# Kernel optimization log

Hardware: AMD Instinct MI355X
Metric: run time of the kernel (lower is better)

Reference implementation:

```python
import jax, jax.numpy as jnp
import numpy as np

B, T, D = 8, 2048, 1024          # batch, seq_len, inp_dim
NH, DH = 8, 128                  # head_num, head_dim
H = NH * DH                      # hidden_dim = 1024
P = int((4.0 / 3.0) * H)         # proj_dim = 1365
EPS = 1e-6
CAP = 15.0                       # soft cap for i/f gate pre-activations


def setup_inputs() -> dict:
    key = jax.random.key(0)
    ks = jax.random.split(key, 32)
    r = lambda k, s, sc=0.02: jax.random.normal(k, s, jnp.float32) * sc
    return {
        "x": jax.random.normal(ks[0], (B, T, D), jnp.float32),
        "ln_w": jnp.ones((D,), jnp.float32),
        "ln_b": jnp.zeros((D,), jnp.float32),
        "hln_w": jnp.ones((H,), jnp.float32),
        "hln_b": jnp.zeros((H,), jnp.float32),
        "Wz": r(ks[1], (D, H)), "bz": r(ks[2], (H,)),
        "Wi": r(ks[3], (D, H)), "bi": r(ks[4], (H,)),
        "Wo": r(ks[5], (D, H)), "bo": r(ks[6], (H,)),
        "Wf": r(ks[7], (D, H)), "bf": r(ks[8], (H,)),
        "Rz": r(ks[9], (NH, DH, DH)), "rbz": r(ks[10], (H,)),
        "Ri": r(ks[11], (NH, DH, DH)), "rbi": r(ks[12], (H,)),
        "Ro": r(ks[13], (NH, DH, DH)), "rbo": r(ks[14], (H,)),
        "Rf": r(ks[15], (NH, DH, DH)), "rbf": r(ks[16], (H,)),
        "up_w": r(ks[17], (H, 2 * P)), "up_b": r(ks[18], (2 * P,)),
        "down_w": r(ks[19], (P, D)), "down_b": r(ks[20], (D,)),
    }


def _layernorm(v, w, b):
    mu = jnp.mean(v, axis=-1, keepdims=True)
    var = jnp.mean((v - mu) ** 2, axis=-1, keepdims=True)
    return (v - mu) * jax.lax.rsqrt(var + EPS) * w + b


def _soft_cap(v):
    return CAP * jnp.tanh(v / CAP)


def _block_linear(h, R, rb):
    # block-diagonal linear: h (B,H) -> per-head (B,NH,DH) @ (NH,DH,DH)
    hh = h.reshape(h.shape[0], NH, DH)
    return jnp.einsum('bhd,hde->bhe', hh, R).reshape(h.shape[0], H) + rb


def _multihead_layernorm(h, w, b):
    hh = h.reshape(h.shape[0], NH, DH)
    mu = jnp.mean(hh, axis=-1, keepdims=True)
    var = jnp.mean((hh - mu) ** 2, axis=-1, keepdims=True)
    normed = (hh - mu) * jax.lax.rsqrt(var + EPS)
    return normed.reshape(h.shape[0], H) * w + b


def reference(x, ln_w, ln_b, hln_w, hln_b,
              Wz, bz, Wi, bi, Wo, bo, Wf, bf,
              Rz, rbz, Ri, rbi, Ro, rbo, Rf, rbf,
              up_w, up_b, down_w, down_b):
    # use_conv=False path: x_c == x_t == LayerNorm(x)
    x_n = _layernorm(x, ln_w, ln_b)                       # (B,T,D)
    # precompute all input projections as large GEMMs
    zx = jnp.einsum('btd,dh->bth', x_n, Wz) + bz
    ix = jnp.einsum('btd,dh->bth', x_n, Wi) + bi
    ox = jnp.einsum('btd,dh->bth', x_n, Wo) + bo
    fx = jnp.einsum('btd,dh->bth', x_n, Wf) + bf

    tm = lambda a: jnp.transpose(a, (1, 0, 2))            # time-major
    xs = (tm(zx), tm(ix), tm(ox), tm(fx), tm(x))

    c0 = jnp.zeros((x.shape[0], H), jnp.float32)
    n0 = jnp.ones((x.shape[0], H), jnp.float32)
    h0 = jnp.zeros((x.shape[0], H), jnp.float32)
    m0 = jnp.zeros((x.shape[0], H), jnp.float32)

    def step(carry, inp_t):
        c, n, h, m = carry
        zx_t, ix_t, ox_t, fx_t, xres_t = inp_t
        i_pre = _soft_cap(ix_t + _block_linear(h, Ri, rbi))
        f_pre = _soft_cap(fx_t + _block_linear(h, Rf, rbf))
        z = jnp.tanh(zx_t + _block_linear(h, Rz, rbz))
        o = jax.nn.sigmoid(ox_t + _block_linear(h, Ro, rbo))
        m_t = jnp.maximum(f_pre + m, i_pre)
        i_g = jnp.exp(i_pre - m_t)
        f_g = jnp.exp(f_pre - m_t + m)
        c_t = f_g * c + i_g * z
        n_t = f_g * n + i_g
        h_t = o * (c_t / jnp.maximum(n_t, 1.0))
        out = _multihead_layernorm(h_t, hln_w, hln_b)
        u = out @ up_w + up_b
        u1, u2 = u[:, :P], u[:, P:]
        y = (u1 * jax.nn.gelu(u2, approximate=False)) @ down_w + down_b
        return (c_t, n_t, h_t, m_t), y + xres_t

    _, ys = jax.lax.scan(step, (c0, n0, h0, m0), xs)      # (T,B,D)
    return jnp.transpose(ys, (1, 0, 2))                   # (B,T,D)
```

## Files before the change

### kernel.cpp

```cpp
#include <hip/hip_runtime.h>

typedef unsigned short u16;
typedef __attribute__((ext_vector_type(4))) float v4f;
typedef __attribute__((ext_vector_type(8))) short bf16x8;

#define B_ 8
#define T_ 2048
#define D_ 1024
#define NH_ 8
#define DH_ 128
#define H_ 1024
#define P_ 1365
#define PPAD_ 1408
#define M_ 16384

__device__ __forceinline__ u16 f2b(float f) {
    union { float f; unsigned u; } v; v.f = f;
    unsigned r = (v.u + 0x7fffu + ((v.u >> 16) & 1u)) >> 16;
    return (u16)r;
}
__device__ __forceinline__ float b2f(u16 u) {
    union { unsigned u; float f; } v; v.u = ((unsigned)u) << 16;
    return v.f;
}

template<int S>
__device__ __forceinline__ float qb(float x) {
    return __int_as_float(__builtin_amdgcn_update_dpp(
        0, __float_as_int(x), S * 0x55, 0xF, 0xF, true));
}

#define GLD16(gp, lp) __builtin_amdgcn_global_load_lds( \
    (const __attribute__((address_space(1))) void*)(gp), \
    (__attribute__((address_space(3))) void*)(lp), 16, 0, 0)

__global__ __launch_bounds__(256) void transpose_cast(
    const float* __restrict__ in, u16* __restrict__ out,
    int K, int N, int Kpad, int Npad, int ldin, int rowmul, int rowoff)
{
    __shared__ float tile[32][33];
    const int tx = threadIdx.x, ty = threadIdx.y;
    const int nblk = blockIdx.x * 32, kblk = blockIdx.y * 32;
#pragma unroll
    for (int i = 0; i < 4; ++i) {
        int k = kblk + ty + i * 8, n = nblk + tx;
        float v = (k < K && n < N) ? in[(size_t)k * ldin + n] : 0.f;
        tile[ty + i * 8][tx] = v;
    }
    __syncthreads();
#pragma unroll
    for (int i = 0; i < 4; ++i) {
        int n = nblk + ty + i * 8, k = kblk + tx;
        if (n < Npad && k < Kpad)
            out[((size_t)n * rowmul + rowoff) * Kpad + k] = f2b(tile[tx][ty + i * 8]);
    }
}

__global__ __launch_bounds__(256) void bias4_concat(
    const float* __restrict__ bz, const float* __restrict__ bi,
    const float* __restrict__ bo, const float* __restrict__ bf,
    float* __restrict__ b4)
{
    int j = blockIdx.x * 256 + threadIdx.x;
    const float* p = (j < 1024) ? bz : (j < 2048) ? bi : (j < 3072) ? bo : bf;
    b4[((j & 1023) << 2) | (j >> 10)] = p[j & 1023];
}

__global__ __launch_bounds__(128) void rq_prep(
    const float* __restrict__ Rz, const float* __restrict__ Ri,
    const float* __restrict__ Ro, const float* __restrict__ Rf,
    u16* __restrict__ RQ)
{
    const int m = blockIdx.x;
    const int hd = blockIdx.y;
    const int d = threadIdx.x;
    const int g = m & 3, e = m >> 2;
    const float* Rg = (g == 0) ? Rz : (g == 1) ? Ri : (g == 2) ? Ro : Rf;
    RQ[((size_t)hd * 512 + m) * 128 + d] =
        f2b(Rg[((size_t)hd * 128 + d) * 128 + e]);
}

__global__ __launch_bounds__(256) void ln_cast_kernel(
    const float* __restrict__ x, const float* __restrict__ w,
    const float* __restrict__ b, u16* __restrict__ xnb)
{
    const int token = blockIdx.x, tid = threadIdx.x;
    const float4* xr = (const float4*)(x + (size_t)token * D_);
    float4 v = xr[tid];
    float s  = v.x + v.y + v.z + v.w;
    float ss = v.x * v.x + v.y * v.y + v.z * v.z + v.w * v.w;
    for (int off = 32; off; off >>= 1) { s += __shfl_down(s, off); ss += __shfl_down(ss, off); }
    __shared__ float wsum[4], wsq[4], stats[2];
    const int wave = tid >> 6, lane = tid & 63;
    if (lane == 0) { wsum[wave] = s; wsq[wave] = ss; }
    __syncthreads();
    if (tid == 0) {
        float S = 0.f, SS = 0.f;
        for (int i = 0; i < 4; ++i) { S += wsum[i]; SS += wsq[i]; }
        float mu = S * (1.f / 1024.f);
        float var = SS * (1.f / 1024.f) - mu * mu;
        stats[0] = mu; stats[1] = rsqrtf(var + 1e-6f);
    }
    __syncthreads();
    const float mu = stats[0], rs = stats[1];
    float4 wv = ((const float4*)w)[tid];
    float4 bv = ((const float4*)b)[tid];
    ushort4 o;
    o.x = f2b((v.x - mu) * rs * wv.x + bv.x);
    o.y = f2b((v.y - mu) * rs * wv.y + bv.y);
    o.z = f2b((v.z - mu) * rs * wv.z + bv.z);
    o.w = f2b((v.w - mu) * rs * wv.w + bv.w);
    ((ushort4*)(xnb + (size_t)token * D_))[tid] = o;
}

__device__ __forceinline__ void gemm128_core(
    const u16* __restrict__ A, const u16* __restrict__ BT,
    int K, int m0, int n0, v4f acc[4][4])
{
    __shared__ __align__(16) u16 As[4096];
    __shared__ __align__(16) u16 Bs[4096];
    const int tid = threadIdx.x;
    const int wave = tid >> 6, lane = tid & 63;
    const int wm = wave & 1, wn = wave >> 1;
    const int srow = tid >> 2, sseg = tid & 3;
    const int lm = lane & 15, lq = lane >> 4;

    const u16* gA0 = A  + (size_t)(m0 + srow) * K + sseg * 8;
    const u16* gA1 = gA0 + (size_t)64 * K;
    const u16* gB0 = BT + (size_t)(n0 + srow) * K + sseg * 8;
    const u16* gB1 = gB0 + (size_t)64 * K;
    u16* lA0 = As + wave * 512;
    u16* lA1 = As + 2048 + wave * 512;
    u16* lB0 = Bs + wave * 512;
    u16* lB1 = Bs + 2048 + wave * 512;

    for (int kk = 0; kk < K; kk += 32) {
        GLD16(gA0 + kk, lA0);
        GLD16(gA1 + kk, lA1);
        GLD16(gB0 + kk, lB0);
        GLD16(gB1 + kk, lB1);
        __syncthreads();
        bf16x8 a[4], b[4];
#pragma unroll
        for (int i = 0; i < 4; ++i) {
            a[i] = *(const bf16x8*)(As + (wm * 64 + i * 16 + lm) * 32 + lq * 8);
            b[i] = *(const bf16x8*)(Bs + (wn * 64 + i * 16 + lm) * 32 + lq * 8);
        }
#pragma unroll
        for (int i = 0; i < 4; ++i)
#pragma unroll
            for (int j = 0; j < 4; ++j)
                acc[i][j] = __builtin_amdgcn_mfma_f32_16x16x32_bf16(a[i], b[j], acc[i][j], 0, 0, 0);
        __syncthreads();
    }
}

__global__ __launch_bounds__(256) void gemm_gate4(
    const u16* __restrict__ A, const u16* __restrict__ WT4,
    const float* __restrict__ bias4, u16* __restrict__ gx4,
    int t0, int Tc)
{
    v4f acc[4][4];
#pragma unroll
    for (int i = 0; i < 4; ++i)
#pragma unroll
        for (int j = 0; j < 4; ++j)
#pragma unroll
            for (int r = 0; r < 4; ++r) acc[i][j][r] = 0.f;
    const int mtPerB = Tc >> 7;
    const int b_ = blockIdx.y / mtPerB, tt = blockIdx.y % mtPerB;
    const int m0 = b_ * T_ + t0 + tt * 128;
    const int n0 = blockIdx.x * 128;
    gemm128_core(A, WT4, D_, m0, n0, acc);
    const int r0 = b_ * Tc + tt * 128;
    const int tid = threadIdx.x, wave = tid >> 6, lane = tid & 63;
    const int wm = wave & 1, wn = wave >> 1;
    const int col = lane & 15, rb0 = (lane >> 4) * 4;
#pragma unroll
    for (int j = 0; j < 4; ++j) {
        const int n = n0 + wn * 64 + j * 16 + col;
        const float bv = bias4[n];
#pragma unroll
        for (int i = 0; i < 4; ++i)
#pragma unroll
            for (int r = 0; r < 4; ++r) {
                const int rr = r0 + wm * 64 + i * 16 + rb0 + r;
                gx4[(size_t)rr * 4096 + n] = f2b(acc[i][j][r] + bv);
            }
    }
}

__global__ __launch_bounds__(512, 1) void scan_kernel(
    const u16* __restrict__ gx4,
    const u16* __restrict__ RQ,
    const float* __restrict__ rb4,
    float* __restrict__ state,
    u16* __restrict__ hraw,
    int t0, int Tc, int init)
{
    const int blk = blockIdx.x;
    const int b = blk >> 3, hd = blk & 7;
    const int tid = threadIdx.x;
    const int w = tid >> 6, lane = tid & 63;
    const int lm = lane & 15, lq = lane >> 4;
    const int g = lane & 3;
    const int e = (w << 4) + (lane >> 2);
    const bool st_lane = (g == 0);

    __shared__ __align__(16) u16 hL[2][128];

    bf16x8 rq[4][4];
    const u16* RQh = RQ + (size_t)hd * (512 * 128);
#pragma unroll
    for (int i = 0; i < 4; ++i)
#pragma unroll
        for (int kc = 0; kc < 4; ++kc)
            rq[i][kc] = *(const bf16x8*)(RQh +
                (size_t)(w * 64 + i * 16 + lm) * 128 + kc * 32 + lq * 8);

    const float K0 = (g == 1 || g == 3) ? 15.f : 1.f;
    const float K1 = (g == 0) ? 2.f : (g == 2) ? 1.f : 30.f;
    const float K2 = (g == 0) ? 2.f : (g == 2) ? 1.f : (2.f / 15.f);
    const float rb_l = rb4[(hd << 9) + (w << 6) + lane];

    float cS = 0.f, nS = 1.f, mS = 0.f, hS = 0.f;
    if (st_lane && !init) {
        float4 s = ((const float4*)state)[(blk << 7) + e];
        cS = s.x; nS = s.y; mS = s.z; hS = s.w;
    }

    if (st_lane) hL[0][e] = f2b(hS);
    __syncthreads();

    const u16* gxb = gx4 + (size_t)b * Tc * 4096 + (hd << 9) + (w << 6) + lane;
    u16* houtp = hraw + (size_t)(b * T_ + t0) * H_ + (hd << 7) + e;

    u16 pgA = gxb[0], pgB = gxb[4096], pgC = gxb[2 * 4096], pgD = gxb[3 * 4096];

#define SCAN_STEP(TL, RB, WB, PG)                                              \
    {                                                                          \
          \
        const bf16x8 hv0 = *(const bf16x8*)(&hL[RB][0 * 32 + lq * 8]);         \
        const bf16x8 hv1 = *(const bf16x8*)(&hL[RB][1 * 32 + lq * 8]);         \
        const bf16x8 hv2 = *(const bf16x8*)(&hL[RB][2 * 32 + lq * 8]);         \
        const bf16x8 hv3 = *(const bf16x8*)(&hL[RB][3 * 32 + lq * 8]);         \
        v4f p0[4], p1[4];                                                      \
        _Pragma("unroll") for (int i = 0; i < 4; ++i)                          \
            _Pragma("unroll") for (int r = 0; r < 4; ++r) {                    \
                p0[i][r] = 0.f; p1[i][r] = 0.f; }                              \
        _Pragma("unroll") for (int i = 0; i < 4; ++i) {                        \
            p0[i] = __builtin_amdgcn_mfma_f32_16x16x32_bf16(hv0, rq[i][0], p0[i], 0, 0, 0); \
            p1[i] = __builtin_amdgcn_mfma_f32_16x16x32_bf16(hv1, rq[i][1], p1[i], 0, 0, 0); \
            p0[i] = __builtin_amdgcn_mfma_f32_16x16x32_bf16(hv2, rq[i][2], p0[i], 0, 0, 0); \
            p1[i] = __builtin_amdgcn_mfma_f32_16x16x32_bf16(hv3, rq[i][3], p1[i], 0, 0, 0); \
        }                                                                      \
        const float s0 = p0[0][0] + p1[0][0];                                  \
        const float s1 = p0[1][0] + p1[1][0];                                  \
        const float s2 = p0[2][0] + p1[2][0];                                  \
        const float s3 = p0[3][0] + p1[3][0];                                  \
        const float sel = (lq & 2) ? ((lq & 1) ? s3 : s2)                      \
                                   : ((lq & 1) ? s1 : s0);                     \
        const int tn = ((TL) + 4 < Tc) ? (TL) + 4 : Tc - 1;                    \
        const u16 pgn = gxb[(size_t)tn * 4096];                                \
        const float pre = sel + b2f(PG) + rb_l;                                \
        PG = pgn;                                                              \
        const float tt = K0 - K1 * __builtin_amdgcn_rcpf(__expf(pre * K2) + 1.f); \
        const float ipv = qb<1>(tt);                                           \
        const float ovv = qb<2>(tt);                                           \
        const float fpv = qb<3>(tt);                                           \
        if (st_lane) {                                                         \
            const float bm = fpv + mS;                                         \
            const float d  = ipv - bm;                                         \
            const float mt = fmaxf(bm, ipv);                                   \
            const float e1 = __expf(-fabsf(d));                                \
            const float ig = (d >= 0.f) ? 1.f : e1;                            \
            const float fg = (d >= 0.f) ? e1 : 1.f;                            \
            cS = fg * cS + ig * tt;                                            \
            nS = fg * nS + ig;                                                 \
            mS = mt;                                                           \
            const float hv = ovv * cS * __builtin_amdgcn_rcpf(fmaxf(nS, 1.f)); \
            hS = hv;                                                           \
            const u16 hb = f2b(hv);                                            \
            hL[WB][e] = hb;                                                    \
            houtp[(size_t)(TL) * H_] = hb;                                     \
        }                                                                      \
        asm volatile("s_waitcnt lgkmcnt(0)" ::: "memory");                     \
        __builtin_amdgcn_s_barrier();                                          \
        __builtin_amdgcn_sched_barrier(0);                                     \
    }

    for (int tl = 0; tl < Tc; tl += 4) {
        SCAN_STEP(tl,     0, 1, pgA)
        SCAN_STEP(tl + 1, 1, 0, pgB)
        SCAN_STEP(tl + 2, 0, 1, pgC)
        SCAN_STEP(tl + 3, 1, 0, pgD)
    }
#undef SCAN_STEP

    if (st_lane) {
        ((float4*)state)[(blk << 7) + e] = make_float4(cS, nS, mS, hS);
    }
}

__global__ __launch_bounds__(512) void mln_kernel(
    const u16* __restrict__ h_all, const float* __restrict__ w,
    const float* __restrict__ b, u16* __restrict__ hb)
{
    const int token = blockIdx.x, tid = threadIdx.x;
    const int wave = tid >> 6, lane = tid & 63;
    const u16* hr = h_all + (size_t)token * H_ + wave * DH_;
    float a0 = b2f(hr[lane]), a1 = b2f(hr[64 + lane]);
    float s = a0 + a1, ss = a0 * a0 + a1 * a1;
    for (int off = 32; off; off >>= 1) { s += __shfl_xor(s, off); ss += __shfl_xor(ss, off); }
    const float mu = s * (1.f / 128.f);
    const float var = ss * (1.f / 128.f) - mu * mu;
    const float rs = rsqrtf(var + 1e-6f);
    const int c0 = wave * DH_ + lane;
    u16* hw = hb + (size_t)token * H_ + wave * DH_;
    hw[lane]      = f2b((a0 - mu) * rs * w[c0] + b[c0]);
    hw[64 + lane] = f2b((a1 - mu) * rs * w[c0 + 64] + b[c0 + 64]);
}

__global__ __launch_bounds__(256) void gemm_up_geglu(
    const u16* __restrict__ A, const u16* __restrict__ B1T,
    const u16* __restrict__ B2T, const float* __restrict__ upb,
    u16* __restrict__ G)
{
    __shared__ __align__(16) u16 As[4096], B1s[4096], B2s[4096];
    v4f acc1[4][4], acc2[4][4];
#pragma unroll
    for (int i = 0; i < 4; ++i)
#pragma unroll
        for (int j = 0; j < 4; ++j)
#pragma unroll
            for (int r = 0; r < 4; ++r) { acc1[i][j][r] = 0.f; acc2[i][j][r] = 0.f; }
    const int m0 = blockIdx.y * 128, n0 = blockIdx.x * 128;
    const int tid = threadIdx.x;
    const int wave = tid >> 6, lane = tid & 63;
    const int wm = wave & 1, wn = wave >> 1;
    const int srow = tid >> 2, sseg = tid & 3;
    const int lm = lane & 15, lq = lane >> 4;

    const u16* gA0 = A   + (size_t)(m0 + srow) * H_ + sseg * 8;
    const u16* gA1 = gA0 + (size_t)64 * H_;
    const u16* g10 = B1T + (size_t)(n0 + srow) * H_ + sseg * 8;
    const u16* g11 = g10 + (size_t)64 * H_;
    const u16* g20 = B2T + (size_t)(n0 + srow) * H_ + sseg * 8;
    const u16* g21 = g20 + (size_t)64 * H_;
    u16* lA0 = As  + wave * 512;        u16* lA1 = As  + 2048 + wave * 512;
    u16* l10 = B1s + wave * 512;        u16* l11 = B1s + 2048 + wave * 512;
    u16* l20 = B2s + wave * 512;        u16* l21 = B2s + 2048 + wave * 512;

    for (int kk = 0; kk < H_; kk += 32) {
        GLD16(gA0 + kk, lA0); GLD16(gA1 + kk, lA1);
        GLD16(g10 + kk, l10); GLD16(g11 + kk, l11);
        GLD16(g20 + kk, l20); GLD16(g21 + kk, l21);
        __syncthreads();
        bf16x8 a[4], b1[4], b2[4];
#pragma unroll
        for (int i = 0; i < 4; ++i) {
            a[i]  = *(const bf16x8*)(As  + (wm * 64 + i * 16 + lm) * 32 + lq * 8);
            b1[i] = *(const bf16x8*)(B1s + (wn * 64 + i * 16 + lm) * 32 + lq * 8);
            b2[i] = *(const bf16x8*)(B2s + (wn * 64 + i * 16 + lm) * 32 + lq * 8);
        }
#pragma unroll
        for (int i = 0; i < 4; ++i)
#pragma unroll
            for (int j = 0; j < 4; ++j) {
                acc1[i][j] = __builtin_amdgcn_mfma_f32_16x16x32_bf16(a[i], b1[j], acc1[i][j], 0, 0, 0);
                acc2[i][j] = __builtin_amdgcn_mfma_f32_16x16x32_bf16(a[i], b2[j], acc2[i][j], 0, 0, 0);
            }
        __syncthreads();
    }
    const int col = lane & 15, rb0 = (lane >> 4) * 4;
#pragma unroll
    for (int j = 0; j < 4; ++j) {
        const int n = n0 + wn * 64 + j * 16 + col;
        const bool ok = (n < P_);
        const float bb1 = ok ? upb[n] : 0.f;
        const float bb2 = ok ? upb[P_ + n] : 0.f;
#pragma unroll
        for (int i = 0; i < 4; ++i)
#pragma unroll
            for (int r = 0; r < 4; ++r) {
                const int mm = m0 + wm * 64 + i * 16 + rb0 + r;
                float gval = 0.f;
                if (ok) {
                    const float u1 = acc1[i][j][r] + bb1;
                    const float u2 = acc2[i][j][r] + bb2;
                    const float ge = 0.5f * u2 * (1.f + erff(u2 * 0.70710678118654752f));
                    gval = u1 * ge;
                }
                G[(size_t)mm * PPAD_ + n] = f2b(gval);
            }
    }
}

__global__ __launch_bounds__(256) void gemm_down_out(
    const u16* __restrict__ A, const u16* __restrict__ BT,
    const float* __restrict__ bias, const float* __restrict__ resid,
    float* __restrict__ C, int K, int ldc)
{
    v4f acc[4][4];
#pragma unroll
    for (int i = 0; i < 4; ++i)
#pragma unroll
        for (int j = 0; j < 4; ++j)
#pragma unroll
            for (int r = 0; r < 4; ++r) acc[i][j][r] = 0.f;
    const int m0 = blockIdx.y * 128, n0 = blockIdx.x * 128;
    gemm128_core(A, BT, K, m0, n0, acc);
    const int tid = threadIdx.x, wave = tid >> 6, lane = tid & 63;
    const int wm = wave & 1, wn = wave >> 1;
    const int col = lane & 15, rb0 = (lane >> 4) * 4;
#pragma unroll
    for (int j = 0; j < 4; ++j) {
        const int n = n0 + wn * 64 + j * 16 + col;
        const float bv = bias[n];
#pragma unroll
        for (int i = 0; i < 4; ++i)
#pragma unroll
            for (int r = 0; r < 4; ++r) {
                const int mm = m0 + wm * 64 + i * 16 + rb0 + r;
                C[(size_t)mm * ldc + n] = acc[i][j][r] + bv + resid[(size_t)mm * ldc + n];
            }
    }
}

extern "C" void kernel_launch(void* const* d_in, const int* in_sizes, int n_in,
                              void* d_out, int out_size, void* d_ws, size_t ws_size,
                              hipStream_t stream)
{
    const float* x     = (const float*)d_in[0];
    const float* ln_w  = (const float*)d_in[1];
    const float* ln_b  = (const float*)d_in[2];
    const float* hln_w = (const float*)d_in[3];
    const float* hln_b = (const float*)d_in[4];
    const float* Wz = (const float*)d_in[5];  const float* bz  = (const float*)d_in[6];
    const float* Wi = (const float*)d_in[7];  const float* bi  = (const float*)d_in[8];
    const float* Wo = (const float*)d_in[9];  const float* bo  = (const float*)d_in[10];
    const float* Wf = (const float*)d_in[11]; const float* bfv = (const float*)d_in[12];
    const float* Rz = (const float*)d_in[13]; const float* rbz = (const float*)d_in[14];
    const float* Ri = (const float*)d_in[15]; const float* rbi = (const float*)d_in[16];
    const float* Ro = (const float*)d_in[17]; const float* rbo = (const float*)d_in[18];
    const float* Rf = (const float*)d_in[19]; const float* rbf = (const float*)d_in[20];
    const float* up_w   = (const float*)d_in[21]; const float* up_b   = (const float*)d_in[22];
    const float* down_w = (const float*)d_in[23]; const float* down_b = (const float*)d_in[24];
    float* out = (float*)d_out;

    size_t off = 0;
    char* base = (char*)d_ws;
    auto alloc = [&](size_t bytes) -> char* {
        char* r = base + off; off += (bytes + 255) & ~(size_t)255; return r;
    };
    u16*   WT4   = (u16*)  alloc((size_t)4 * H_ * D_ * 2);
    u16*   W1T   = (u16*)  alloc((size_t)PPAD_ * H_ * 2);
    u16*   W2T   = (u16*)  alloc((size_t)PPAD_ * H_ * 2);
    u16*   dnT   = (u16*)  alloc((size_t)D_ * PPAD_ * 2);
    u16*   RQ    = (u16*)  alloc((size_t)8 * 512 * 128 * 2);
    float* bias4 = (float*)alloc(4096 * 4);
    float* rb4   = (float*)alloc(4096 * 4);
    float* state = (float*)alloc((size_t)64 * 4 * 128 * 4);
    u16*   hbn   = (u16*)  alloc((size_t)M_ * H_ * 2);
    char*  dyn   = base + off;
    u16*   xnb   = (u16*)dyn;
    const size_t xnb_bytes = (size_t)M_ * H_ * 2;
    u16*   gbuf  = (u16*)dyn;

    const size_t fixed = off + xnb_bytes;
    int Tc = 256;
    if      (ws_size >= fixed + (size_t)4 * B_ * 2048 * H_ * 2) Tc = 2048;
    else if (ws_size >= fixed + (size_t)4 * B_ * 1024 * H_ * 2) Tc = 1024;
    else if (ws_size >= fixed + (size_t)4 * B_ * 512  * H_ * 2) Tc = 512;
    u16* gx = (u16*)(dyn + xnb_bytes);
    const int NC = T_ / Tc;

    dim3 tb(32, 8);
    const float* Ws[4] = {Wz, Wi, Wo, Wf};
    for (int g = 0; g < 4; ++g)
        transpose_cast<<<dim3(32, 32), tb, 0, stream>>>(
            Ws[g], WT4, D_, H_, D_, H_, H_, 4, g);
    transpose_cast<<<dim3(44, 32), tb, 0, stream>>>(up_w,      W1T, H_, P_, H_, PPAD_, 2 * P_, 1, 0);
    transpose_cast<<<dim3(44, 32), tb, 0, stream>>>(up_w + P_, W2T, H_, P_, H_, PPAD_, 2 * P_, 1, 0);
    transpose_cast<<<dim3(32, 44), tb, 0, stream>>>(down_w, dnT, P_, D_, PPAD_, D_, D_, 1, 0);
    bias4_concat<<<16, 256, 0, stream>>>(bz, bi, bo, bfv, bias4);
    bias4_concat<<<16, 256, 0, stream>>>(rbz, rbi, rbo, rbf, rb4);
    rq_prep<<<dim3(512, 8), 128, 0, stream>>>(Rz, Ri, Ro, Rf, RQ);

    ln_cast_kernel<<<M_, 256, 0, stream>>>(x, ln_w, ln_b, xnb);

    for (int cidx = 0; cidx < NC; ++cidx) {
        const int t0 = cidx * Tc;
        gemm_gate4<<<dim3(32, B_ * (Tc / 128)), 256, 0, stream>>>(
            xnb, WT4, bias4, gx, t0, Tc);
        scan_kernel<<<64, 512, 0, stream>>>(
            gx, RQ, rb4, state, hbn, t0, Tc, cidx == 0 ? 1 : 0);
    }

    mln_kernel<<<M_, 512, 0, stream>>>(hbn, hln_w, hln_b, hbn);

    gemm_up_geglu<<<dim3(PPAD_ / 128, 128), 256, 0, stream>>>(hbn, W1T, W2T, up_b, gbuf);
    gemm_down_out<<<dim3(8, 128), 256, 0, stream>>>(gbuf, dnT, down_b, x, out, PPAD_, D_);

    (void)in_sizes; (void)n_in; (void)out_size;
}
```

Baseline: 1.601 ms.

## Fuse gate GEMM and recurrent scan into one persistent kernel with flag handoff

Replaces the separate gate-projection GEMM launch and scan launch with one kernel. The first 64 blocks run the recurrence and the remaining 192 blocks compute gate pre-activation tiles. Each finished 128-row tile bumps a per-(batch, time-tile) counter, and scan blocks spin on these counters so the sequential scan can start while later tiles are still being produced. It also drops the explicit zeroing of MFMA accumulators in the scan step. The scheme relies on all 256 blocks being co-resident, since spin-waiting deadlocks otherwise, and the GEMM tiles now use 512 threads with a 128x256 tile shape.

Result: slower. 1.724 ms (+7.7%).

```diff
diff --git a/kernel.cpp b/kernel.cpp
--- a/kernel.cpp
+++ b/kernel.cpp
@@ -13,6 +13,9 @@
 #define P_ 1365
 #define PPAD_ 1408
 #define M_ 16384
+
+#define NSCAN 64
+#define NGEMM 192
 
 __device__ __forceinline__ u16 f2b(float f) {
     union { float f; unsigned u; } v; v.f = f;
@@ -155,60 +158,99 @@
     }
 }
 
-__global__ __launch_bounds__(256) void gemm_gate4(
-    const u16* __restrict__ A, const u16* __restrict__ WT4,
-    const float* __restrict__ bias4, u16* __restrict__ gx4,
-    int t0, int Tc)
-{
-    v4f acc[4][4];
-#pragma unroll
-    for (int i = 0; i < 4; ++i)
-#pragma unroll
-        for (int j = 0; j < 4; ++j)
-#pragma unroll
-            for (int r = 0; r < 4; ++r) acc[i][j][r] = 0.f;
-    const int mtPerB = Tc >> 7;
-    const int b_ = blockIdx.y / mtPerB, tt = blockIdx.y % mtPerB;
-    const int m0 = b_ * T_ + t0 + tt * 128;
-    const int n0 = blockIdx.x * 128;
-    gemm128_core(A, WT4, D_, m0, n0, acc);
-    const int r0 = b_ * Tc + tt * 128;
-    const int tid = threadIdx.x, wave = tid >> 6, lane = tid & 63;
-    const int wm = wave & 1, wn = wave >> 1;
-    const int col = lane & 15, rb0 = (lane >> 4) * 4;
-#pragma unroll
-    for (int j = 0; j < 4; ++j) {
-        const int n = n0 + wn * 64 + j * 16 + col;
-        const float bv = bias4[n];
-#pragma unroll
-        for (int i = 0; i < 4; ++i)
-#pragma unroll
-            for (int r = 0; r < 4; ++r) {
-                const int rr = r0 + wm * 64 + i * 16 + rb0 + r;
-                gx4[(size_t)rr * 4096 + n] = f2b(acc[i][j][r] + bv);
-            }
-    }
-}
-
-__global__ __launch_bounds__(512, 1) void scan_kernel(
-    const u16* __restrict__ gx4,
+__global__ __launch_bounds__(512, 1) void fused_gemm_scan(
+    const u16* __restrict__ xnb,
+    const u16* __restrict__ WT4,
+    const float* __restrict__ bias4,
+    u16* __restrict__ gx4,
     const u16* __restrict__ RQ,
     const float* __restrict__ rb4,
     float* __restrict__ state,
     u16* __restrict__ hraw,
+    unsigned* __restrict__ flags,
     int t0, int Tc, int init)
 {
+    const int tid = threadIdx.x;
+
+    __shared__ __align__(16) u16 As[128 * 32];
+    __shared__ __align__(16) u16 Bs[256 * 32];
+    __shared__ __align__(16) u16 hL[2][128];
+
+    if (blockIdx.x >= NSCAN) {
+        const int gb = blockIdx.x - NSCAN;
+        const int wave = tid >> 6, lane = tid & 63;
+        const int wm = wave & 1, wn = wave >> 1;
+        const int lm = lane & 15, lq = lane >> 4;
+        const int srow = tid >> 2, sseg = tid & 3;
+        const int RT = (Tc >> 7) * B_;
+        const int TT = RT << 4;
+        for (int gti = gb; gti < TT; gti += NGEMM) {
+            const int rtp = gti >> 4, nt = gti & 15;
+            const int tt = rtp >> 3, b = rtp & 7;
+            const int m0 = b * T_ + t0 + (tt << 7);
+            const int r0 = b * Tc + (tt << 7);
+            const int n0 = nt << 8;
+            v4f acc[4][4];
+#pragma unroll
+            for (int i = 0; i < 4; ++i)
+#pragma unroll
+                for (int j = 0; j < 4; ++j)
+#pragma unroll
+                    for (int r = 0; r < 4; ++r) acc[i][j][r] = 0.f;
+            const u16* gA  = xnb + (size_t)(m0 + srow) * D_ + sseg * 8;
+            const u16* gB0 = WT4 + (size_t)(n0 + srow) * D_ + sseg * 8;
+            const u16* gB1 = WT4 + (size_t)(n0 + 128 + srow) * D_ + sseg * 8;
+            u16* lA  = As + wave * 512;
+            u16* lB0 = Bs + wave * 512;
+            u16* lB1 = Bs + 4096 + wave * 512;
+            for (int kk = 0; kk < D_; kk += 32) {
+                GLD16(gA + kk, lA);
+                GLD16(gB0 + kk, lB0);
+                GLD16(gB1 + kk, lB1);
+                __syncthreads();
+                bf16x8 av[4], bv[4];
+#pragma unroll
+                for (int i = 0; i < 4; ++i) {
+                    av[i] = *(const bf16x8*)(As + (wm * 64 + i * 16 + lm) * 32 + lq * 8);
+                    bv[i] = *(const bf16x8*)(Bs + (wn * 64 + i * 16 + lm) * 32 + lq * 8);
+                }
+#pragma unroll
+                for (int i = 0; i < 4; ++i)
+#pragma unroll
+                    for (int j = 0; j < 4; ++j)
+                        acc[i][j] = __builtin_amdgcn_mfma_f32_16x16x32_bf16(av[i], bv[j], acc[i][j], 0, 0, 0);
+                __syncthreads();
+            }
+            const int col = lm, rb0 = lq * 4;
+#pragma unroll
+            for (int j = 0; j < 4; ++j) {
+                const int n = n0 + wn * 64 + j * 16 + col;
+                const float bvv = bias4[n];
+#pragma unroll
+                for (int i = 0; i < 4; ++i)
+#pragma unroll
+                    for (int r = 0; r < 4; ++r) {
+                        const int rr = r0 + wm * 64 + i * 16 + rb0 + r;
+                        gx4[(size_t)rr * 4096 + n] = f2b(acc[i][j][r] + bvv);
+                    }
+            }
+            __syncthreads();
+            if (tid == 0) {
+                __threadfence();
+                atomicAdd(&flags[(b << 4) + (t0 >> 7) + tt], 1u);
+            }
+        }
+        return;
+    }
+
     const int blk = blockIdx.x;
     const int b = blk >> 3, hd = blk & 7;
-    const int tid = threadIdx.x;
     const int w = tid >> 6, lane = tid & 63;
     const int lm = lane & 15, lq = lane >> 4;
     const int g = lane & 3;
     const int e = (w << 4) + (lane >> 2);
     const bool st_lane = (g == 0);
 
-    __shared__ __align__(16) u16 hL[2][128];
-
     bf16x8 rq[4][4];
     const u16* RQh = RQ + (size_t)hd * (512 * 128);
 #pragma unroll
@@ -230,12 +272,24 @@
     }
 
     if (st_lane) hL[0][e] = f2b(hS);
+
+    const int gtt0 = (t0 >> 7);
+    const int smax = (Tc >> 7) - 1;
+    const unsigned* fb = flags + (b << 4) + gtt0;
+
+    if (tid == 0) {
+        while (__hip_atomic_load(&fb[0], __ATOMIC_RELAXED,
+                                 __HIP_MEMORY_SCOPE_AGENT) < 16u) {}
+    }
     __syncthreads();
+    __threadfence();
 
     const u16* gxb = gx4 + (size_t)b * Tc * 4096 + (hd << 9) + (w << 6) + lane;
     u16* houtp = hraw + (size_t)(b * T_ + t0) * H_ + (hd << 7) + e;
 
     u16 pgA = gxb[0], pgB = gxb[4096], pgC = gxb[2 * 4096], pgD = gxb[3 * 4096];
+
+    const v4f z4 = {0.f, 0.f, 0.f, 0.f};
 
 #define SCAN_STEP(TL, RB, WB, PG)                                              \
     {                                                                          \
@@ -245,12 +299,9 @@
         const bf16x8 hv2 = *(const bf16x8*)(&hL[RB][2 * 32 + lq * 8]);         \
         const bf16x8 hv3 = *(const bf16x8*)(&hL[RB][3 * 32 + lq * 8]);         \
         v4f p0[4], p1[4];                                                      \
-        _Pragma("unroll") for (int i = 0; i < 4; ++i)                          \
-            _Pragma("unroll") for (int r = 0; r < 4; ++r) {                    \
-                p0[i][r] = 0.f; p1[i][r] = 0.f; }                              \
         _Pragma("unroll") for (int i = 0; i < 4; ++i) {                        \
-            p0[i] = __builtin_amdgcn_mfma_f32_16x16x32_bf16(hv0, rq[i][0], p0[i], 0, 0, 0); \
-            p1[i] = __builtin_amdgcn_mfma_f32_16x16x32_bf16(hv1, rq[i][1], p1[i], 0, 0, 0); \
+            p0[i] = __builtin_amdgcn_mfma_f32_16x16x32_bf16(hv0, rq[i][0], z4, 0, 0, 0); \
+            p1[i] = __builtin_amdgcn_mfma_f32_16x16x32_bf16(hv1, rq[i][1], z4, 0, 0, 0); \
             p0[i] = __builtin_amdgcn_mfma_f32_16x16x32_bf16(hv2, rq[i][2], p0[i], 0, 0, 0); \
             p1[i] = __builtin_amdgcn_mfma_f32_16x16x32_bf16(hv3, rq[i][3], p1[i], 0, 0, 0); \
         }                                                                      \
@@ -264,10 +315,10 @@
         const u16 pgn = gxb[(size_t)tn * 4096];                                \
         const float pre = sel + b2f(PG) + rb_l;                                \
         PG = pgn;                                                              \
-        const float tt = K0 - K1 * __builtin_amdgcn_rcpf(__expf(pre * K2) + 1.f); \
-        const float ipv = qb<1>(tt);                                           \
-        const float ovv = qb<2>(tt);                                           \
-        const float fpv = qb<3>(tt);                                           \
+        const float tt_ = K0 - K1 * __builtin_amdgcn_rcpf(__expf(pre * K2) + 1.f); \
+        const float ipv = qb<1>(tt_);                                          \
+        const float ovv = qb<2>(tt_);                                          \
+        const float fpv = qb<3>(tt_);                                          \
         if (st_lane) {                                                         \
             const float bm = fpv + mS;                                         \
             const float d  = ipv - bm;                                         \
@@ -275,10 +326,11 @@
             const float e1 = __expf(-fabsf(d));                                \
             const float ig = (d >= 0.f) ? 1.f : e1;                            \
             const float fg = (d >= 0.f) ? e1 : 1.f;                            \
-            cS = fg * cS + ig * tt;                                            \
             nS = fg * nS + ig;                                                 \
+            const float rp = __builtin_amdgcn_rcpf(fmaxf(nS, 1.f));            \
+            cS = fg * cS + ig * tt_;                                           \
             mS = mt;                                                           \
-            const float hv = ovv * cS * __builtin_amdgcn_rcpf(fmaxf(nS, 1.f)); \
+            const float hv = ovv * cS * rp;                                    \
             hS = hv;                                                           \
             const u16 hb = f2b(hv);                                            \
             hL[WB][e] = hb;                                                    \
@@ -289,11 +341,22 @@
         __builtin_amdgcn_sched_barrier(0);                                     \
     }
 
-    for (int tl = 0; tl < Tc; tl += 4) {
-        SCAN_STEP(tl,     0, 1, pgA)
-        SCAN_STEP(tl + 1, 1, 0, pgB)
-        SCAN_STEP(tl + 2, 0, 1, pgC)
-        SCAN_STEP(tl + 3, 1, 0, pgD)
+    for (int s = 0; s <= smax; ++s) {
+        const int wtt = (s + 1 <= smax) ? s + 1 : smax;
+        if (tid == 0) {
+            while (__hip_atomic_load(&fb[wtt], __ATOMIC_RELAXED,
+                                     __HIP_MEMORY_SCOPE_AGENT) < 16u) {}
+        }
+        __syncthreads();
+        __threadfence();
+        const int base = s << 7;
+        for (int tl4 = 0; tl4 < 128; tl4 += 4) {
+            const int tl = base + tl4;
+            SCAN_STEP(tl,     0, 1, pgA)
+            SCAN_STEP(tl + 1, 1, 0, pgB)
+            SCAN_STEP(tl + 2, 0, 1, pgC)
+            SCAN_STEP(tl + 3, 1, 0, pgD)
+        }
     }
 #undef SCAN_STEP
 
@@ -461,6 +524,7 @@
     float* bias4 = (float*)alloc(4096 * 4);
     float* rb4   = (float*)alloc(4096 * 4);
     float* state = (float*)alloc((size_t)64 * 4 * 128 * 4);
+    unsigned* flags = (unsigned*)alloc(128 * 4);
     u16*   hbn   = (u16*)  alloc((size_t)M_ * H_ * 2);
     char*  dyn   = base + off;
     u16*   xnb   = (u16*)dyn;
@@ -474,6 +538,8 @@
     else if (ws_size >= fixed + (size_t)4 * B_ * 512  * H_ * 2) Tc = 512;
     u16* gx = (u16*)(dyn + xnb_bytes);
     const int NC = T_ / Tc;
+
+    hipMemsetAsync(flags, 0, 128 * 4, stream);
 
     dim3 tb(32, 8);
     const float* Ws[4] = {Wz, Wi, Wo, Wf};
@@ -491,10 +557,9 @@
 
     for (int cidx = 0; cidx < NC; ++cidx) {
         const int t0 = cidx * Tc;
-        gemm_gate4<<<dim3(32, B_ * (Tc / 128)), 256, 0, stream>>>(
-            xnb, WT4, bias4, gx, t0, Tc);
-        scan_kernel<<<64, 512, 0, stream>>>(
-            gx, RQ, rb4, state, hbn, t0, Tc, cidx == 0 ? 1 : 0);
+        fused_gemm_scan<<<NSCAN + NGEMM, 512, 0, stream>>>(
+            xnb, WT4, bias4, gx, RQ, rb4, state, hbn, flags,
+            t0, Tc, cidx == 0 ? 1 : 0);
     }
 
     mln_kernel<<<M_, 512, 0, stream>>>(hbn, hln_w, hln_b, hbn);
```

## Widen gate and down GEMM tiles to 128x256 and add XCD-aware block swizzle

Applied to the files above, without the earlier changes.

Replaces the shared 128x128 GEMM core with 512-thread kernels whose 8 waves cover a 128x256 output tile. Each A tile loaded into LDS now feeds twice as many output columns. All three big GEMMs (gate, up-GeGLU, down) also get a 1-D grid with a remap that groups consecutive tiles onto the same XCD, aiming for better L2 reuse of the A rows. The cost is fewer blocks per GEMM, more LDS per block, and more threads contending at each barrier.

Result: no change. 1.612 ms (+0.7%).

```diff
diff --git a/kernel.cpp b/kernel.cpp
--- a/kernel.cpp
+++ b/kernel.cpp
@@ -28,6 +28,12 @@
 __device__ __forceinline__ float qb(float x) {
     return __int_as_float(__builtin_amdgcn_update_dpp(
         0, __float_as_int(x), S * 0x55, 0xF, 0xF, true));
+}
+
+__device__ __forceinline__ int xcd_swz(int bid, int nwg) {
+    const int xcd = bid & 7, idx = bid >> 3;
+    const int q = nwg >> 3, r = nwg & 7;
+    return (xcd < r ? xcd * (q + 1) : r * (q + 1) + (xcd - r) * q) + idx;
 }
 
 #define GLD16(gp, lp) __builtin_amdgcn_global_load_lds( \
@@ -113,53 +119,29 @@
     ((ushort4*)(xnb + (size_t)token * D_))[tid] = o;
 }
 
-__device__ __forceinline__ void gemm128_core(
-    const u16* __restrict__ A, const u16* __restrict__ BT,
-    int K, int m0, int n0, v4f acc[4][4])
-{
-    __shared__ __align__(16) u16 As[4096];
-    __shared__ __align__(16) u16 Bs[4096];
-    const int tid = threadIdx.x;
-    const int wave = tid >> 6, lane = tid & 63;
-    const int wm = wave & 1, wn = wave >> 1;
-    const int srow = tid >> 2, sseg = tid & 3;
-    const int lm = lane & 15, lq = lane >> 4;
-
-    const u16* gA0 = A  + (size_t)(m0 + srow) * K + sseg * 8;
-    const u16* gA1 = gA0 + (size_t)64 * K;
-    const u16* gB0 = BT + (size_t)(n0 + srow) * K + sseg * 8;
-    const u16* gB1 = gB0 + (size_t)64 * K;
-    u16* lA0 = As + wave * 512;
-    u16* lA1 = As + 2048 + wave * 512;
-    u16* lB0 = Bs + wave * 512;
-    u16* lB1 = Bs + 2048 + wave * 512;
-
-    for (int kk = 0; kk < K; kk += 32) {
-        GLD16(gA0 + kk, lA0);
-        GLD16(gA1 + kk, lA1);
-        GLD16(gB0 + kk, lB0);
-        GLD16(gB1 + kk, lB1);
-        __syncthreads();
-        bf16x8 a[4], b[4];
-#pragma unroll
-        for (int i = 0; i < 4; ++i) {
-            a[i] = *(const bf16x8*)(As + (wm * 64 + i * 16 + lm) * 32 + lq * 8);
-            b[i] = *(const bf16x8*)(Bs + (wn * 64 + i * 16 + lm) * 32 + lq * 8);
-        }
-#pragma unroll
-        for (int i = 0; i < 4; ++i)
-#pragma unroll
-            for (int j = 0; j < 4; ++j)
-                acc[i][j] = __builtin_amdgcn_mfma_f32_16x16x32_bf16(a[i], b[j], acc[i][j], 0, 0, 0);
-        __syncthreads();
-    }
-}
-
-__global__ __launch_bounds__(256) void gemm_gate4(
+__global__ __launch_bounds__(512) void gemm_gate4_w(
     const u16* __restrict__ A, const u16* __restrict__ WT4,
     const float* __restrict__ bias4, u16* __restrict__ gx4,
     int t0, int Tc)
 {
+    __shared__ __align__(16) u16 As[4096];
+    __shared__ __align__(16) u16 Bs[8192];
+    const int tid = threadIdx.x;
+    const int mtPerB = Tc >> 7;
+    const int MT = B_ * mtPerB;
+    const int nwg = MT * 16;
+    const int sid = xcd_swz(blockIdx.x, nwg);
+    const int nt = sid / MT, mt = sid % MT;
+    const int b_ = mt / mtPerB, tt = mt % mtPerB;
+    const int m0 = b_ * T_ + t0 + tt * 128;
+    const int r0 = b_ * Tc + tt * 128;
+    const int n0 = nt << 8;
+
+    const int wave = tid >> 6, lane = tid & 63;
+    const int wm = wave & 1, wn = wave >> 1;
+    const int lm = lane & 15, lq = lane >> 4;
+    const int srow = tid >> 2, sseg = tid & 3;
+
     v4f acc[4][4];
 #pragma unroll
     for (int i = 0; i < 4; ++i)
@@ -167,25 +149,40 @@
         for (int j = 0; j < 4; ++j)
 #pragma unroll
             for (int r = 0; r < 4; ++r) acc[i][j][r] = 0.f;
-    const int mtPerB = Tc >> 7;
-    const int b_ = blockIdx.y / mtPerB, tt = blockIdx.y % mtPerB;
-    const int m0 = b_ * T_ + t0 + tt * 128;
-    const int n0 = blockIdx.x * 128;
-    gemm128_core(A, WT4, D_, m0, n0, acc);
-    const int r0 = b_ * Tc + tt * 128;
-    const int tid = threadIdx.x, wave = tid >> 6, lane = tid & 63;
-    const int wm = wave & 1, wn = wave >> 1;
-    const int col = lane & 15, rb0 = (lane >> 4) * 4;
+
+    const u16* gA  = A   + (size_t)(m0 + srow) * D_ + sseg * 8;
+    const u16* gB0 = WT4 + (size_t)(n0 + srow) * D_ + sseg * 8;
+    const u16* gB1 = WT4 + (size_t)(n0 + 128 + srow) * D_ + sseg * 8;
+    u16* lA  = As + wave * 512;
+    u16* lB0 = Bs + wave * 512;
+    u16* lB1 = Bs + 4096 + wave * 512;
+
+    for (int kk = 0; kk < D_; kk += 32) {
+        GLD16(gA + kk, lA); GLD16(gB0 + kk, lB0); GLD16(gB1 + kk, lB1);
+        __syncthreads();
+        bf16x8 av[4], bv[4];
+#pragma unroll
+        for (int i = 0; i < 4; ++i) {
+            av[i] = *(const bf16x8*)(As + (wm * 64 + i * 16 + lm) * 32 + lq * 8);
+            bv[i] = *(const bf16x8*)(Bs + (wn * 64 + i * 16 + lm) * 32 + lq * 8);
+        }
+#pragma unroll
+        for (int i = 0; i < 4; ++i)
+#pragma unroll
+            for (int j = 0; j < 4; ++j)
+                acc[i][j] = __builtin_amdgcn_mfma_f32_16x16x32_bf16(av[i], bv[j], acc[i][j], 0, 0, 0);
+        __syncthreads();
+    }
 #pragma unroll
     for (int j = 0; j < 4; ++j) {
-        const int n = n0 + wn * 64 + j * 16 + col;
-        const float bv = bias4[n];
+        const int n = n0 + wn * 64 + j * 16 + lm;
+        const float bvv = bias4[n];
 #pragma unroll
         for (int i = 0; i < 4; ++i)
 #pragma unroll
             for (int r = 0; r < 4; ++r) {
-                const int rr = r0 + wm * 64 + i * 16 + rb0 + r;
-                gx4[(size_t)rr * 4096 + n] = f2b(acc[i][j][r] + bv);
+                const int rr = r0 + wm * 64 + i * 16 + lq * 4 + r;
+                gx4[(size_t)rr * 4096 + n] = f2b(acc[i][j][r] + bvv);
             }
     }
 }
@@ -239,7 +236,6 @@
 
 #define SCAN_STEP(TL, RB, WB, PG)                                              \
     {                                                                          \
-          \
         const bf16x8 hv0 = *(const bf16x8*)(&hL[RB][0 * 32 + lq * 8]);         \
         const bf16x8 hv1 = *(const bf16x8*)(&hL[RB][1 * 32 + lq * 8]);         \
         const bf16x8 hv2 = *(const bf16x8*)(&hL[RB][2 * 32 + lq * 8]);         \
@@ -264,10 +260,10 @@
         const u16 pgn = gxb[(size_t)tn * 4096];                                \
         const float pre = sel + b2f(PG) + rb_l;                                \
         PG = pgn;                                                              \
-        const float tt = K0 - K1 * __builtin_amdgcn_rcpf(__expf(pre * K2) + 1.f); \
-        const float ipv = qb<1>(tt);                                           \
-        const float ovv = qb<2>(tt);                                           \
-        const float fpv = qb<3>(tt);                                           \
+        const float tt_ = K0 - K1 * __builtin_amdgcn_rcpf(__expf(pre * K2) + 1.f); \
+        const float ipv = qb<1>(tt_);                                          \
+        const float ovv = qb<2>(tt_);                                          \
+        const float fpv = qb<3>(tt_);                                          \
         if (st_lane) {                                                         \
             const float bm = fpv + mS;                                         \
             const float d  = ipv - bm;                                         \
@@ -275,7 +271,7 @@
             const float e1 = __expf(-fabsf(d));                                \
             const float ig = (d >= 0.f) ? 1.f : e1;                            \
             const float fg = (d >= 0.f) ? e1 : 1.f;                            \
-            cS = fg * cS + ig * tt;                                            \
+            cS = fg * cS + ig * tt_;                                           \
             nS = fg * nS + ig;                                                 \
             mS = mt;                                                           \
             const float hv = ovv * cS * __builtin_amdgcn_rcpf(fmaxf(nS, 1.f)); \
@@ -334,7 +330,9 @@
         for (int j = 0; j < 4; ++j)
 #pragma unroll
             for (int r = 0; r < 4; ++r) { acc1[i][j][r] = 0.f; acc2[i][j][r] = 0.f; }
-    const int m0 = blockIdx.y * 128, n0 = blockIdx.x * 128;
+    const int nwg = (PPAD_ / 128) * 128;
+    const int sid = xcd_swz(blockIdx.x, nwg);
+    const int n0 = (sid / 128) * 128, m0 = (sid % 128) * 128;
     const int tid = threadIdx.x;
     const int wave = tid >> 6, lane = tid & 63;
     const int wm = wave & 1, wn = wave >> 1;
@@ -396,11 +394,24 @@
     }
 }
 
-__global__ __launch_bounds__(256) void gemm_down_out(
-    const u16* __restrict__ A, const u16* __restrict__ BT,
+__global__ __launch_bounds__(512) void gemm_down_w(
+    const u16* __restrict__ A,
+    const u16* __restrict__ BT,
     const float* __restrict__ bias, const float* __restrict__ resid,
-    float* __restrict__ C, int K, int ldc)
-{
+    float* __restrict__ C)
+{
+    __shared__ __align__(16) u16 As[4096];
+    __shared__ __align__(16) u16 Bs[8192];
+    const int tid = threadIdx.x;
+    const int nwg = 4 * 128;
+    const int sid = xcd_swz(blockIdx.x, nwg);
+    const int n0 = (sid >> 7) << 8, m0 = (sid & 127) << 7;
+
+    const int wave = tid >> 6, lane = tid & 63;
+    const int wm = wave & 1, wn = wave >> 1;
+    const int lm = lane & 15, lq = lane >> 4;
+    const int srow = tid >> 2, sseg = tid & 3;
+
     v4f acc[4][4];
 #pragma unroll
     for (int i = 0; i < 4; ++i)
@@ -408,21 +419,40 @@
         for (int j = 0; j < 4; ++j)
 #pragma unroll
             for (int r = 0; r < 4; ++r) acc[i][j][r] = 0.f;
-    const int m0 = blockIdx.y * 128, n0 = blockIdx.x * 128;
-    gemm128_core(A, BT, K, m0, n0, acc);
-    const int tid = threadIdx.x, wave = tid >> 6, lane = tid & 63;
-    const int wm = wave & 1, wn = wave >> 1;
-    const int col = lane & 15, rb0 = (lane >> 4) * 4;
+
+    const u16* gA  = A  + (size_t)(m0 + srow) * PPAD_ + sseg * 8;
+    const u16* gB0 = BT + (size_t)(n0 + srow) * PPAD_ + sseg * 8;
+    const u16* gB1 = BT + (size_t)(n0 + 128 + srow) * PPAD_ + sseg * 8;
+    u16* lA  = As + wave * 512;
+    u16* lB0 = Bs + wave * 512;
+    u16* lB1 = Bs + 4096 + wave * 512;
+
+    for (int kk = 0; kk < PPAD_; kk += 32) {
+        GLD16(gA + kk, lA); GLD16(gB0 + kk, lB0); GLD16(gB1 + kk, lB1);
+        __syncthreads();
+        bf16x8 av[4], bv[4];
+#pragma unroll
+        for (int i = 0; i < 4; ++i) {
+            av[i] = *(const bf16x8*)(As + (wm * 64 + i * 16 + lm) * 32 + lq * 8);
+            bv[i] = *(const bf16x8*)(Bs + (wn * 64 + i * 16 + lm) * 32 + lq * 8);
+        }
+#pragma unroll
+        for (int i = 0; i < 4; ++i)
+#pragma unroll
+            for (int j = 0; j < 4; ++j)
+                acc[i][j] = __builtin_amdgcn_mfma_f32_16x16x32_bf16(av[i], bv[j], acc[i][j], 0, 0, 0);
+        __syncthreads();
+    }
 #pragma unroll
     for (int j = 0; j < 4; ++j) {
-        const int n = n0 + wn * 64 + j * 16 + col;
+        const int n = n0 + wn * 64 + j * 16 + lm;
         const float bv = bias[n];
 #pragma unroll
         for (int i = 0; i < 4; ++i)
 #pragma unroll
             for (int r = 0; r < 4; ++r) {
-                const int mm = m0 + wm * 64 + i * 16 + rb0 + r;
-                C[(size_t)mm * ldc + n] = acc[i][j][r] + bv + resid[(size_t)mm * ldc + n];
+                const int mm = m0 + wm * 64 + i * 16 + lq * 4 + r;
+                C[(size_t)mm * D_ + n] = acc[i][j][r] + bv + resid[(size_t)mm * D_ + n];
             }
     }
 }
@@ -491,7 +521,7 @@
 
     for (int cidx = 0; cidx < NC; ++cidx) {
         const int t0 = cidx * Tc;
-        gemm_gate4<<<dim3(32, B_ * (Tc / 128)), 256, 0, stream>>>(
+        gemm_gate4_w<<<B_ * (Tc / 128) * 16, 512, 0, stream>>>(
             xnb, WT4, bias4, gx, t0, Tc);
         scan_kernel<<<64, 512, 0, stream>>>(
             gx, RQ, rb4, state, hbn, t0, Tc, cidx == 0 ? 1 : 0);
@@ -499,8 +529,8 @@
 
     mln_kernel<<<M_, 512, 0, stream>>>(hbn, hln_w, hln_b, hbn);
 
-    gemm_up_geglu<<<dim3(PPAD_ / 128, 128), 256, 0, stream>>>(hbn, W1T, W2T, up_b, gbuf);
-    gemm_down_out<<<dim3(8, 128), 256, 0, stream>>>(gbuf, dnT, down_b, x, out, PPAD_, D_);
+    gemm_up_geglu<<<(PPAD_ / 128) * 128, 256, 0, stream>>>(hbn, W1T, W2T, up_b, gbuf);
+    gemm_down_w<<<4 * 128, 512, 0, stream>>>(gbuf, dnT, down_b, x, out);
 
     (void)in_sizes; (void)n_in; (void)out_size;
 }
```
